# Kernel tuning notes

Measured on AMD Instinct MI355X. Metric: run time of the kernel, lower is better.

Reference implementation:

```python
import math
import jax, jax.numpy as jnp
import numpy as np

T, B, IN, H, D, ETA, R = 128, 32, 512, 8, 64, 4, 4
DE = ETA * D  # expanded key dim = eta * head_dim
EPS = 1e-05


def setup_inputs() -> dict:
    key = jax.random.key(0)
    ks = jax.random.split(key, 8)
    s = 0.05
    return {
        "inputs": jax.random.normal(ks[0], (T, B, IN), jnp.float32),
        "terminations": jnp.zeros((T, B), jnp.float32),
        "tilde_k_prev": jax.random.normal(ks[1], (B, R, H, DE), jnp.float32) * s,
        "tilde_v_prev": jax.random.normal(ks[2], (B, R, H, D), jnp.float32) * s,
        "s_prev": jax.random.normal(ks[3], (B, H, DE), jnp.float32) * s,
        "tick": jnp.zeros((B, 1), jnp.float32),
        "W_kqv": jax.random.normal(ks[4], (H * D * 5, IN), jnp.float32) * s,
        "b_kqv": jnp.zeros((H * D * 5,), jnp.float32),
        "W_p": jax.random.normal(ks[5], (H * ETA * 3, IN), jnp.float32) * s,
        "b_p": jnp.zeros((H * ETA * 3,), jnp.float32),
        "W_o": jax.random.normal(ks[6], (IN, H * D), jnp.float32) * s,
        "b_o": jnp.zeros((IN,), jnp.float32),
    }


def _forward(inputs, terminations, tilde_k_prev, tilde_v_prev, s_prev, tick,
             W_kqv, b_kqv, W_p, b_p, W_o, b_o):
    # projections
    kqv = (inputs @ W_kqv.T + b_kqv).reshape(T, B, H, 5, D)
    keys, queries, values, beta, gammas = (kqv[..., i, :] for i in range(5))
    p = (inputs @ W_p.T + b_p).reshape(T, B, H, 3, ETA)
    p1, p2, p3 = (p[..., i, :] for i in range(3))
    relu, sig = jax.nn.relu, jax.nn.sigmoid
    # kernel feature maps: outer product then flatten (d outer, n inner)
    keys = jnp.einsum('tbhd,tbhn->tbhdn', relu(keys), relu(p1)).reshape(T, B, H, DE)
    queries = jnp.einsum('tbhd,tbhn->tbhdn', relu(queries), relu(p2)).reshape(T, B, H, DE)
    gammas = jnp.einsum('tbhd,tbhn->tbhdn', sig(gammas), sig(p3)).reshape(T, B, H, DE)
    beta = sig(beta)  # (T,B,H,D)
    # oscillatory basis
    ticks = tick[None] + jnp.arange(1, T + 1, dtype=jnp.float32).reshape(T, 1, 1)  # (T,B,1)
    omegas = jnp.linspace(-math.pi, math.pi, R)
    occil = jnp.cos(ticks * omegas[None, None, :])  # (T,B,R)
    values = values * beta
    values_r = values[:, :, None] * occil[:, :, :, None, None]   # (T,B,R,H,D)
    keys_g = keys * gammas                                        # (T,B,H,DE)
    keys_r = keys_g[:, :, None] * occil[:, :, :, None, None]     # (T,B,R,H,DE)
    # discounts (with termination resets)
    nt = (1.0 - terminations)[:, :, None, None]
    dg = (1.0 - gammas) * nt  # (T,B,H,DE)
    db = (1.0 - beta) * nt    # (T,B,H,D)
    # recurrence y[t] = discount[t]*y[t-1] + x[t] via lax.scan over T
    def step(carry, xs):
        k_st, v_st, s_st = carry
        kx, vx, sx, dgt, dbt = xs
        k_new = dgt[:, None] * k_st + kx   # (B,R,H,DE)
        v_new = dbt[:, None] * v_st + vx   # (B,R,H,D)
        s_new = dgt * s_st + sx            # (B,H,DE)
        return (k_new, v_new, s_new), (k_new, v_new, s_new)
    (kf, vf, sf), (K, V, S) = jax.lax.scan(
        step, (tilde_k_prev, tilde_v_prev, s_prev), (keys_r, values_r, keys_g, dg, db))
    # attention readout
    kdq = jnp.einsum('tbrhd,tbhd->tbrh', K, queries)
    kv = jnp.einsum('tbrhd,tbrh->tbhd', V, kdq)
    norm = jnp.einsum('tbhd,tbhd->tbh', S, queries)
    attn = kv / (2 * R * norm[..., None] + EPS)  # (T,B,H,D)
    out = attn.reshape(T, B, H * D) @ W_o.T + b_o  # dropout p=0 (eval)
    return out, kf, vf, sf, tick + T


def reference(inputs, terminations, tilde_k_prev, tilde_v_prev, s_prev, tick,
              W_kqv, b_kqv, W_p, b_p, W_o, b_o):
    return _forward(inputs, terminations, tilde_k_prev, tilde_v_prev, s_prev, tick,
                    W_kqv, b_kqv, W_p, b_p, W_o, b_o)
```

## Files before the change

kernel.cpp:

```cpp
#include <hip/hip_runtime.h>
#include <math.h>
#include <stdint.h>

constexpr int T_ = 128, B_ = 32, IN_ = 512, H_ = 8, D_ = 64, ETA_ = 4, R_ = 4;
constexpr int DE_ = ETA_ * D_;
constexpr float EPS_ = 1e-5f;
constexpr int NKQV = H_ * 5 * D_;
constexpr int NP   = H_ * 3 * ETA_;
constexpr int M_   = T_ * B_;
constexpr int NCH  = 8;
constexpr int CH   = T_ / NCH;
constexpr int BH_  = B_ * H_;

typedef __attribute__((ext_vector_type(8))) short bf16x8;
typedef __attribute__((ext_vector_type(4))) float f32x4;

__device__ __forceinline__ float bf2f(unsigned short u) {
    return __builtin_bit_cast(float, ((unsigned)u) << 16);
}
__device__ __forceinline__ unsigned short f2bf(float f) {
    unsigned u = __builtin_bit_cast(unsigned, f);
    u = (u + 0x7fffu + ((u >> 16) & 1u)) >> 16;
    return (unsigned short)u;
}
__device__ __forceinline__ float fsigm(float x) {
    return __fdividef(1.f, 1.f + __expf(-x));
}

__global__ __launch_bounds__(256) void cast_f32_bf16(
    const float* __restrict__ src, unsigned short* __restrict__ dst, int n8)
{
    int i = blockIdx.x * 256 + threadIdx.x;
    if (i >= n8) return;
    const float4* s = (const float4*)src;
    float4 a = s[2 * i], b = s[2 * i + 1];
    *(ushort4*)(dst + 8 * i)     = make_ushort4(f2bf(a.x), f2bf(a.y), f2bf(a.z), f2bf(a.w));
    *(ushort4*)(dst + 8 * i + 4) = make_ushort4(f2bf(b.x), f2bf(b.y), f2bf(b.z), f2bf(b.w));
}

__global__ __launch_bounds__(256) void cast_split(
    const float* __restrict__ src, unsigned short* __restrict__ dst,
    int n4, int K3, int off_lo, int off_hi2)
{
    int i = blockIdx.x * 256 + threadIdx.x;
    if (i >= n4) return;
    const int r = i >> 7;
    const int c = (i & 127) << 2;
    float4 x = *(const float4*)(src + (size_t)r * 512 + c);
    ushort4 hi = make_ushort4(f2bf(x.x), f2bf(x.y), f2bf(x.z), f2bf(x.w));
    ushort4 lo = make_ushort4(f2bf(x.x - bf2f(hi.x)), f2bf(x.y - bf2f(hi.y)),
                              f2bf(x.z - bf2f(hi.z)), f2bf(x.w - bf2f(hi.w)));
    unsigned short* dr = dst + (size_t)r * K3 + c;
    *(ushort4*)dr = hi;
    *(ushort4*)(dr + off_lo) = lo;
    if (off_hi2 >= 0) *(ushort4*)(dr + off_hi2) = hi;
}

__device__ __forceinline__ void gl_lds16(const unsigned short* g, unsigned short* l) {
    __builtin_amdgcn_global_load_lds((const __attribute__((address_space(1))) void*)g,
                                     (__attribute__((address_space(3))) void*)l, 16, 0, 0);
}
__device__ __forceinline__ int ko_map(bool split, int ko) {
    return (split && ko >= 512) ? ko - 512 : ko;
}

template <bool SPLIT>
__global__ __launch_bounds__(256) void gemm_bf16(
    const unsigned short* __restrict__ A,
    const unsigned short* __restrict__ W,
    const float* __restrict__ bias1, const float* __restrict__ bias2,
    float* __restrict__ C1, float* __restrict__ C2,
    int M, int N1, int N2, int K, int sA, int sW)
{
    int bx, by;
    {
        const int nwg = gridDim.x * gridDim.y;
        int lin = blockIdx.y * gridDim.x + blockIdx.x;
        lin = (lin & 7) * (nwg >> 3) + (lin >> 3);
        const int G = (gridDim.x % 7 == 0) ? 7 : gridDim.x;
        const int grpsz = gridDim.y * G;
        const int cg = lin / grpsz, rem = lin % grpsz;
        by = rem / G;
        bx = cg * G + rem % G;
    }
    const int Ntot = N1 + N2;
    const int bm = by * 128;
    const int bn = bx * 128;
    const int tid = threadIdx.x;
    const int lane = tid & 63;
    const int wid = tid >> 6;
    const int wr = wid >> 1;
    const int wc = wid & 1;

    __shared__ __align__(16) unsigned short As[2][4096];
    __shared__ __align__(16) unsigned short Bs[2][4096];

    const int arow = tid & 127;
    const int akg  = tid >> 7;
    const unsigned short* aSrc = A + (size_t)(bm + arow) * sA + akg * 8;
    int wrow = bn + arow; if (wrow >= Ntot) wrow = 0;
    const unsigned short* bSrc = W + (size_t)wrow * sW + akg * 8;
    const int gb0 = (wid * 64) * 8;
    const int gb1 = (256 + wid * 64) * 8;

    const int fA = (((lane >> 4) * 128) + wr * 64 + (lane & 15)) * 8;
    const int fB = (((lane >> 4) * 128) + wc * 64 + (lane & 15)) * 8;

    f32x4 acc[4][4] = {};
    const int NKT = K >> 5;

    gl_lds16(aSrc, &As[0][gb0]);
    gl_lds16(aSrc + 16, &As[0][gb1]);
    gl_lds16(bSrc, &Bs[0][gb0]);
    gl_lds16(bSrc + 16, &Bs[0][gb1]);
    __syncthreads();

    for (int kt = 0; kt < NKT; ++kt) {
        const int cur = kt & 1;
        if (kt + 1 < NKT) {
            const int ko  = (kt + 1) << 5;
            const int koA = ko_map(SPLIT, ko);
            gl_lds16(aSrc + koA, &As[cur ^ 1][gb0]);
            gl_lds16(aSrc + koA + 16, &As[cur ^ 1][gb1]);
            gl_lds16(bSrc + ko, &Bs[cur ^ 1][gb0]);
            gl_lds16(bSrc + ko + 16, &Bs[cur ^ 1][gb1]);
        }
        bf16x8 af[4], bfr[4];
#pragma unroll
        for (int m = 0; m < 4; ++m) af[m] = *(const bf16x8*)&As[cur][fA + m * 128];
#pragma unroll
        for (int n = 0; n < 4; ++n) bfr[n] = *(const bf16x8*)&Bs[cur][fB + n * 128];
#pragma unroll
        for (int m = 0; m < 4; ++m)
#pragma unroll
            for (int n = 0; n < 4; ++n)
                acc[m][n] = __builtin_amdgcn_mfma_f32_16x16x32_bf16(af[m], bfr[n], acc[m][n], 0, 0, 0);
        __syncthreads();
    }

#pragma unroll
    for (int n = 0; n < 4; ++n) {
        const int col = bn + wc * 64 + n * 16 + (lane & 15);
        if (col < Ntot) {
            const float bv = (col < N1) ? bias1[col] : bias2[col - N1];
#pragma unroll
            for (int m = 0; m < 4; ++m) {
                const int row0 = bm + wr * 64 + m * 16 + ((lane >> 4) << 2);
#pragma unroll
                for (int j = 0; j < 4; ++j) {
                    const float v = acc[m][n][j] + bv;
                    const int row = row0 + j;
                    if (col < N1)
                        C1[(size_t)row * N1 + col] = v;
                    else
                        C2[(size_t)row * N2 + (col - N1)] = v;
                }
            }
        }
    }
}

template <int CTRL, int RM>
__device__ __forceinline__ float dpp_radd(float x) {
    int t = __builtin_amdgcn_update_dpp(0, __builtin_bit_cast(int, x), CTRL, RM, 0xf, true);
    return x + __builtin_bit_cast(float, t);
}
__device__ __forceinline__ float wave_allsum(float x) {
    x = dpp_radd<0x111, 0xf>(x);
    x = dpp_radd<0x112, 0xf>(x);
    x = dpp_radd<0x114, 0xf>(x);
    x = dpp_radd<0x118, 0xf>(x);
    x = dpp_radd<0x142, 0xa>(x);
    x = dpp_radd<0x143, 0xc>(x);
    return __builtin_bit_cast(float, __builtin_amdgcn_readlane(__builtin_bit_cast(int, x), 63));
}

__device__ __forceinline__ void osc2(float tt, float& oc03, float& oc12) {
    oc03 = cosf(3.14159265358979323846f * tt);
    oc12 = cosf(1.04719755119659774615f * tt);
}


__global__ __launch_bounds__(64) void scanA(
    const float* __restrict__ kqv, const float* __restrict__ pbuf,
    const float* __restrict__ term, const float* __restrict__ tick,
    float* __restrict__ Dg, float* __restrict__ Db,
    float* __restrict__ Kloc, float* __restrict__ Vloc, float* __restrict__ Sloc)
{
    const int bh = blockIdx.x & (BH_ - 1);
    const int c  = blockIdx.x >> 8;
    const int b = bh >> 3, h = bh & 7;
    const int d = threadIdx.x;

    float K0[4] = {}, K1[4] = {}, K2[4] = {}, K3[4] = {}, S[4] = {};
    float V0 = 0.f, V1 = 0.f, V2 = 0.f, V3 = 0.f;
    float Dgv[4] = {1.f, 1.f, 1.f, 1.f};
    float Dbv = 1.f;
    const float tk = tick[b];

    for (int t = c * CH; t < (c + 1) * CH; ++t) {
        const float* kq = kqv + ((size_t)t * B_ + b) * NKQV + h * 320;
        const float c0 = kq[d], c2 = kq[128 + d], c3 = kq[192 + d], c4 = kq[256 + d];
        const float* pr = pbuf + ((size_t)t * B_ + b) * NP + h * 12;
        const float4 p1 = *(const float4*)pr;
        const float4 p3 = *(const float4*)(pr + 8);
        const float nt = 1.f - term[(size_t)t * B_ + b];

        float oc03, oc12; osc2(tk + (float)(t + 1), oc03, oc12);
        const float sgam = fsigm(c4);
        const float rk = fmaxf(c0, 0.f);
        const float sbet = fsigm(c3);
        const float vb = c2 * sbet;
        const float dbv = (1.f - sbet) * nt;
        const float p1a[4] = {p1.x, p1.y, p1.z, p1.w};
        const float p3a[4] = {p3.x, p3.y, p3.z, p3.w};
#pragma unroll
        for (int n = 0; n < 4; ++n) {
            const float g  = sgam * fsigm(p3a[n]);
            const float kg = rk * fmaxf(p1a[n], 0.f) * g;
            const float dg = (1.f - g) * nt;
            S[n]  = fmaf(dg, S[n],  kg);
            K0[n] = fmaf(dg, K0[n], kg * oc03);
            K1[n] = fmaf(dg, K1[n], kg * oc12);
            K2[n] = fmaf(dg, K2[n], kg * oc12);
            K3[n] = fmaf(dg, K3[n], kg * oc03);
            Dgv[n] *= dg;
        }
        V0 = fmaf(dbv, V0, vb * oc03);
        V1 = fmaf(dbv, V1, vb * oc12);
        V2 = fmaf(dbv, V2, vb * oc12);
        V3 = fmaf(dbv, V3, vb * oc03);
        Dbv *= dbv;
    }

    const size_t cb = (size_t)c * BH_ + bh;
    *(float4*)&Dg[cb * DE_ + 4 * d] = make_float4(Dgv[0], Dgv[1], Dgv[2], Dgv[3]);
    Db[cb * D_ + d] = Dbv;
    *(float4*)&Kloc[(cb * 4 + 0) * DE_ + 4 * d] = make_float4(K0[0], K0[1], K0[2], K0[3]);
    *(float4*)&Kloc[(cb * 4 + 1) * DE_ + 4 * d] = make_float4(K1[0], K1[1], K1[2], K1[3]);
    *(float4*)&Kloc[(cb * 4 + 2) * DE_ + 4 * d] = make_float4(K2[0], K2[1], K2[2], K2[3]);
    *(float4*)&Kloc[(cb * 4 + 3) * DE_ + 4 * d] = make_float4(K3[0], K3[1], K3[2], K3[3]);
    Vloc[(cb * 4 + 0) * D_ + d] = V0;
    Vloc[(cb * 4 + 1) * D_ + d] = V1;
    Vloc[(cb * 4 + 2) * D_ + d] = V2;
    Vloc[(cb * 4 + 3) * D_ + d] = V3;
    *(float4*)&Sloc[cb * DE_ + 4 * d] = make_float4(S[0], S[1], S[2], S[3]);
}

__global__ __launch_bounds__(256) void scanB(
    const float* __restrict__ k_prev, const float* __restrict__ v_prev,
    const float* __restrict__ s_prev,
    float* __restrict__ Dg, float* __restrict__ Db,
    float* __restrict__ Kloc, float* __restrict__ Vloc, float* __restrict__ Sloc)
{
    const int bh = blockIdx.x;
    const int b = bh >> 3, h = bh & 7;
    const int de = threadIdx.x;

    float Kin[4], Sin, Vin[4];
#pragma unroll
    for (int r = 0; r < 4; ++r)
        Kin[r] = k_prev[((size_t)(b * 4 + r) * 8 + h) * DE_ + de];
    Sin = s_prev[((size_t)b * 8 + h) * DE_ + de];
    if (de < D_) {
#pragma unroll
        for (int r = 0; r < 4; ++r)
            Vin[r] = v_prev[((size_t)(b * 4 + r) * 8 + h) * D_ + de];
    }

    for (int c = 0; c < NCH; ++c) {
        const size_t cb = (size_t)c * BH_ + bh;
        const float dg = Dg[cb * DE_ + de];
#pragma unroll
        for (int r = 0; r < 4; ++r) {
            const size_t ix = (cb * 4 + r) * DE_ + de;
            const float kl = Kloc[ix];
            Kloc[ix] = Kin[r];
            Kin[r] = fmaf(dg, Kin[r], kl);
        }
        {
            const size_t ix = cb * DE_ + de;
            const float sl = Sloc[ix];
            Sloc[ix] = Sin;
            Sin = fmaf(dg, Sin, sl);
        }
        if (de < D_) {
            const float db = Db[cb * D_ + de];
#pragma unroll
            for (int r = 0; r < 4; ++r) {
                const size_t ix = (cb * 4 + r) * D_ + de;
                const float vl = Vloc[ix];
                Vloc[ix] = Vin[r];
                Vin[r] = fmaf(db, Vin[r], vl);
            }
        }
    }
}

__global__ __launch_bounds__(64) void scanC(
    const float* __restrict__ kqv, const float* __restrict__ pbuf,
    const float* __restrict__ term, const float* __restrict__ tick,
    const float* __restrict__ Kloc, const float* __restrict__ Vloc,
    const float* __restrict__ Sloc,
    unsigned short* __restrict__ attn,
    float* __restrict__ kf, float* __restrict__ vf, float* __restrict__ sf,
    float* __restrict__ tick_out)
{
    const int bh = blockIdx.x & (BH_ - 1);
    const int c  = blockIdx.x >> 8;
    const int b = bh >> 3, h = bh & 7;
    const int d = threadIdx.x;
    const size_t cb = (size_t)c * BH_ + bh;

    float K0[4], K1[4], K2[4], K3[4], S[4];
    float V0, V1, V2, V3;
    {
        float4 k4;
        k4 = *(const float4*)&Kloc[(cb * 4 + 0) * DE_ + 4 * d];
        K0[0] = k4.x; K0[1] = k4.y; K0[2] = k4.z; K0[3] = k4.w;
        k4 = *(const float4*)&Kloc[(cb * 4 + 1) * DE_ + 4 * d];
        K1[0] = k4.x; K1[1] = k4.y; K1[2] = k4.z; K1[3] = k4.w;
        k4 = *(const float4*)&Kloc[(cb * 4 + 2) * DE_ + 4 * d];
        K2[0] = k4.x; K2[1] = k4.y; K2[2] = k4.z; K2[3] = k4.w;
        k4 = *(const float4*)&Kloc[(cb * 4 + 3) * DE_ + 4 * d];
        K3[0] = k4.x; K3[1] = k4.y; K3[2] = k4.z; K3[3] = k4.w;
        k4 = *(const float4*)&Sloc[cb * DE_ + 4 * d];
        S[0] = k4.x; S[1] = k4.y; S[2] = k4.z; S[3] = k4.w;
        V0 = Vloc[(cb * 4 + 0) * D_ + d];
        V1 = Vloc[(cb * 4 + 1) * D_ + d];
        V2 = Vloc[(cb * 4 + 2) * D_ + d];
        V3 = Vloc[(cb * 4 + 3) * D_ + d];
    }
    const float tk = tick[b];

    for (int t = c * CH; t < (c + 1) * CH; ++t) {
        const float* kq = kqv + ((size_t)t * B_ + b) * NKQV + h * 320;
        const float c0 = kq[d], c1 = kq[64 + d], c2 = kq[128 + d],
                    c3 = kq[192 + d], c4 = kq[256 + d];
        const float* pr = pbuf + ((size_t)t * B_ + b) * NP + h * 12;
        const float4 p1 = *(const float4*)pr;
        const float4 p2 = *(const float4*)(pr + 4);
        const float4 p3 = *(const float4*)(pr + 8);
        const float nt = 1.f - term[(size_t)t * B_ + b];

        float oc03, oc12; osc2(tk + (float)(t + 1), oc03, oc12);
        const float sgam = fsigm(c4);
        const float rk = fmaxf(c0, 0.f);
        const float rq = fmaxf(c1, 0.f);
        const float sbet = fsigm(c3);
        const float vb = c2 * sbet;
        const float dbv = (1.f - sbet) * nt;
        const float p1a[4] = {p1.x, p1.y, p1.z, p1.w};
        const float p2a[4] = {p2.x, p2.y, p2.z, p2.w};
        const float p3a[4] = {p3.x, p3.y, p3.z, p3.w};

        float s0 = 0.f, s1 = 0.f, s2 = 0.f, s3 = 0.f, s4 = 0.f;
#pragma unroll
        for (int n = 0; n < 4; ++n) {
            const float g  = sgam * fsigm(p3a[n]);
            const float kg = rk * fmaxf(p1a[n], 0.f) * g;
            const float qe = rq * fmaxf(p2a[n], 0.f);
            const float dg = (1.f - g) * nt;
            S[n]  = fmaf(dg, S[n],  kg);
            K0[n] = fmaf(dg, K0[n], kg * oc03);
            K1[n] = fmaf(dg, K1[n], kg * oc12);
            K2[n] = fmaf(dg, K2[n], kg * oc12);
            K3[n] = fmaf(dg, K3[n], kg * oc03);
            s0 = fmaf(K0[n], qe, s0);
            s1 = fmaf(K1[n], qe, s1);
            s2 = fmaf(K2[n], qe, s2);
            s3 = fmaf(K3[n], qe, s3);
            s4 = fmaf(S[n],  qe, s4);
        }
        V0 = fmaf(dbv, V0, vb * oc03);
        V1 = fmaf(dbv, V1, vb * oc12);
        V2 = fmaf(dbv, V2, vb * oc12);
        V3 = fmaf(dbv, V3, vb * oc03);

        const float kdq0 = wave_allsum(s0);
        const float kdq1 = wave_allsum(s1);
        const float kdq2 = wave_allsum(s2);
        const float kdq3 = wave_allsum(s3);
        const float nrm  = wave_allsum(s4);

        const float kv = V0 * kdq0 + V1 * kdq1 + V2 * kdq2 + V3 * kdq3;
        attn[((size_t)t * B_ + b) * (H_ * D_) + h * D_ + d] =
            f2bf(__fdividef(kv, 2.f * (float)R_ * nrm + EPS_));
    }

    if (c == NCH - 1) {
        *(float4*)&kf[((size_t)(b * 4 + 0) * 8 + h) * DE_ + 4 * d] = make_float4(K0[0], K0[1], K0[2], K0[3]);
        *(float4*)&kf[((size_t)(b * 4 + 1) * 8 + h) * DE_ + 4 * d] = make_float4(K1[0], K1[1], K1[2], K1[3]);
        *(float4*)&kf[((size_t)(b * 4 + 2) * 8 + h) * DE_ + 4 * d] = make_float4(K2[0], K2[1], K2[2], K2[3]);
        *(float4*)&kf[((size_t)(b * 4 + 3) * 8 + h) * DE_ + 4 * d] = make_float4(K3[0], K3[1], K3[2], K3[3]);
        *(float4*)&sf[((size_t)b * 8 + h) * DE_ + 4 * d] = make_float4(S[0], S[1], S[2], S[3]);
        vf[((size_t)(b * 4 + 0) * 8 + h) * D_ + d] = V0;
        vf[((size_t)(b * 4 + 1) * 8 + h) * D_ + d] = V1;
        vf[((size_t)(b * 4 + 2) * 8 + h) * D_ + d] = V2;
        vf[((size_t)(b * 4 + 3) * 8 + h) * D_ + d] = V3;
        if (h == 0 && d == 0) tick_out[b] = tk + (float)T_;
    }
}

extern "C" void kernel_launch(void* const* d_in, const int* in_sizes, int n_in,
                              void* d_out, int out_size, void* d_ws, size_t ws_size,
                              hipStream_t stream)
{
    const float* inputs = (const float*)d_in[0];
    const float* term   = (const float*)d_in[1];
    const float* k_prev = (const float*)d_in[2];
    const float* v_prev = (const float*)d_in[3];
    const float* s_prev = (const float*)d_in[4];
    const float* tick   = (const float*)d_in[5];
    const float* W_kqv  = (const float*)d_in[6];
    const float* b_kqv  = (const float*)d_in[7];
    const float* W_p    = (const float*)d_in[8];
    const float* b_p    = (const float*)d_in[9];
    const float* W_o    = (const float*)d_in[10];
    const float* b_o    = (const float*)d_in[11];

    float* out = (float*)d_out;
    float* kf  = out + (size_t)T_ * B_ * IN_;
    float* vf  = kf  + (size_t)B_ * R_ * H_ * DE_;
    float* sf  = vf  + (size_t)B_ * R_ * H_ * D_;
    float* tick_out = sf + (size_t)B_ * H_ * DE_;

    float* kqv_f  = (float*)d_ws;
    float* p_f    = kqv_f + (size_t)M_ * NKQV;
    unsigned short* attn_bf = (unsigned short*)(p_f + (size_t)M_ * NP);
    unsigned short* Wo_bf   = attn_bf + (size_t)M_ * IN_;
    unsigned short* A2      = Wo_bf + (size_t)IN_ * (H_ * D_);
    unsigned short* W2      = A2 + (size_t)M_ * 1024;

    float* Dg   = (float*)A2;
    float* Db   = Dg   + (size_t)NCH * BH_ * DE_;
    float* Kloc = Db   + (size_t)NCH * BH_ * D_;
    float* Vloc = Kloc + (size_t)NCH * BH_ * 4 * DE_;
    float* Sloc = Vloc + (size_t)NCH * BH_ * 4 * D_;

    {
        int n4 = M_ * 128;
        cast_split<<<(n4 + 255) / 256, 256, 0, stream>>>(inputs, A2, n4, 1024, 512, -1);
        n4 = NKQV * 128;
        cast_split<<<(n4 + 255) / 256, 256, 0, stream>>>(W_kqv, W2, n4, 1536, 512, 1024);
        n4 = NP * 128;
        cast_split<<<(n4 + 255) / 256, 256, 0, stream>>>(W_p, W2 + (size_t)NKQV * 1536, n4, 1536, 512, 1024);
        int n8 = (IN_ * (H_ * D_)) / 8;
        cast_f32_bf16<<<(n8 + 255) / 256, 256, 0, stream>>>(W_o, Wo_bf, n8);
    }

    {
        dim3 grid((NKQV + NP + 127) / 128, M_ / 128);
        gemm_bf16<true><<<grid, 256, 0, stream>>>(A2, W2, b_kqv, b_p,
                                                  kqv_f, p_f, M_, NKQV, NP,
                                                  1536, 1024, 1536);
    }

    scanA<<<NCH * BH_, 64, 0, stream>>>(kqv_f, p_f, term, tick,
                                        Dg, Db, Kloc, Vloc, Sloc);
    scanB<<<BH_, 256, 0, stream>>>(k_prev, v_prev, s_prev,
                                   Dg, Db, Kloc, Vloc, Sloc);
    scanC<<<NCH * BH_, 64, 0, stream>>>(kqv_f, p_f, term, tick,
                                        Kloc, Vloc, Sloc, attn_bf,
                                        kf, vf, sf, tick_out);

    {
        dim3 grid(IN_ / 128, M_ / 128);
        gemm_bf16<false><<<grid, 256, 0, stream>>>(attn_bf, Wo_bf, b_o, b_o,
                                                   out, nullptr, M_, IN_, 0,
                                                   512, 512, 512);
    }
}
```

Measured before the change: 163.5 us.

## Permute projection weights so value/beta columns use single-pass bf16 GEMM

Reorders the kqv/p weight rows into one permuted matrix with a permuted bias, placing keys, queries, gammas and p first, then zero padding, then values and beta. Column tiles before the split column run the 3-term split-bf16 GEMM (K=1536), while value and beta tiles run plain bf16 (K=512). This cuts MFMA work for about 40% of the output columns and merges the two output buffers into one. Values and beta lose the hi/lo precision compensation, which risks accuracy.

```diff
diff --git a/kernel.cpp b/kernel.cpp
--- a/kernel.cpp
+++ b/kernel.cpp
@@ -5,13 +5,14 @@
 constexpr int T_ = 128, B_ = 32, IN_ = 512, H_ = 8, D_ = 64, ETA_ = 4, R_ = 4;
 constexpr int DE_ = ETA_ * D_;
 constexpr float EPS_ = 1e-5f;
-constexpr int NKQV = H_ * 5 * D_;
-constexpr int NP   = H_ * 3 * ETA_;
 constexpr int M_   = T_ * B_;
 constexpr int NCH  = 8;
 constexpr int CH   = T_ / NCH;
 constexpr int BH_  = B_ * H_;
 
+constexpr int NW = 2688;
+constexpr int SPLITCOL = 1664;
+
 typedef __attribute__((ext_vector_type(8))) short bf16x8;
 typedef __attribute__((ext_vector_type(4))) float f32x4;
 
@@ -27,20 +28,8 @@
     return __fdividef(1.f, 1.f + __expf(-x));
 }
 
-__global__ __launch_bounds__(256) void cast_f32_bf16(
-    const float* __restrict__ src, unsigned short* __restrict__ dst, int n8)
-{
-    int i = blockIdx.x * 256 + threadIdx.x;
-    if (i >= n8) return;
-    const float4* s = (const float4*)src;
-    float4 a = s[2 * i], b = s[2 * i + 1];
-    *(ushort4*)(dst + 8 * i)     = make_ushort4(f2bf(a.x), f2bf(a.y), f2bf(a.z), f2bf(a.w));
-    *(ushort4*)(dst + 8 * i + 4) = make_ushort4(f2bf(b.x), f2bf(b.y), f2bf(b.z), f2bf(b.w));
-}
-
-__global__ __launch_bounds__(256) void cast_split(
-    const float* __restrict__ src, unsigned short* __restrict__ dst,
-    int n4, int K3, int off_lo, int off_hi2)
+__global__ __launch_bounds__(256) void cast_splitA(
+    const float* __restrict__ src, unsigned short* __restrict__ dst, int n4)
 {
     int i = blockIdx.x * 256 + threadIdx.x;
     if (i >= n4) return;
@@ -50,27 +39,79 @@
     ushort4 hi = make_ushort4(f2bf(x.x), f2bf(x.y), f2bf(x.z), f2bf(x.w));
     ushort4 lo = make_ushort4(f2bf(x.x - bf2f(hi.x)), f2bf(x.y - bf2f(hi.y)),
                               f2bf(x.z - bf2f(hi.z)), f2bf(x.w - bf2f(hi.w)));
-    unsigned short* dr = dst + (size_t)r * K3 + c;
+    unsigned short* dr = dst + (size_t)r * 1024 + c;
     *(ushort4*)dr = hi;
-    *(ushort4*)(dr + off_lo) = lo;
-    if (off_hi2 >= 0) *(ushort4*)(dr + off_hi2) = hi;
+    *(ushort4*)(dr + 512) = lo;
+}
+
+__global__ __launch_bounds__(256) void build_w2_bias(
+    const float* __restrict__ Wkqv, const float* __restrict__ Wp,
+    const float* __restrict__ bkqv, const float* __restrict__ bp,
+    unsigned short* __restrict__ W2, float* __restrict__ bias_perm)
+{
+    int i = blockIdx.x * 256 + threadIdx.x;
+    if (i >= NW * 128) return;
+    const int rr = i >> 7;
+    const int c = (i & 127) << 2;
+
+    bool zero = false;
+    const float* srow = nullptr;
+    float bv = 0.f;
+    if (rr < 512) {
+        const int h = rr >> 6, dd = rr & 63, s = h * 320 + dd;
+        srow = Wkqv + (size_t)s * 512; bv = bkqv[s];
+    } else if (rr < 1024) {
+        const int q = rr - 512, h = q >> 6, dd = q & 63, s = h * 320 + 64 + dd;
+        srow = Wkqv + (size_t)s * 512; bv = bkqv[s];
+    } else if (rr < 1536) {
+        const int q = rr - 1024, h = q >> 6, dd = q & 63, s = h * 320 + 256 + dd;
+        srow = Wkqv + (size_t)s * 512; bv = bkqv[s];
+    } else if (rr < 1632) {
+        const int q = rr - 1536;
+        srow = Wp + (size_t)q * 512; bv = bp[q];
+    } else if (rr < 1664) {
+        zero = true;
+    } else if (rr < 2176) {
+        const int q = rr - 1664, h = q >> 6, dd = q & 63, s = h * 320 + 128 + dd;
+        srow = Wkqv + (size_t)s * 512; bv = bkqv[s];
+    } else {
+        const int q = rr - 2176, h = q >> 6, dd = q & 63, s = h * 320 + 192 + dd;
+        srow = Wkqv + (size_t)s * 512; bv = bkqv[s];
+    }
+
+    float4 x = zero ? make_float4(0.f, 0.f, 0.f, 0.f) : *(const float4*)(srow + c);
+    ushort4 hi = make_ushort4(f2bf(x.x), f2bf(x.y), f2bf(x.z), f2bf(x.w));
+    ushort4 lo = make_ushort4(f2bf(x.x - bf2f(hi.x)), f2bf(x.y - bf2f(hi.y)),
+                              f2bf(x.z - bf2f(hi.z)), f2bf(x.w - bf2f(hi.w)));
+    unsigned short* dr = W2 + (size_t)rr * 1536 + c;
+    *(ushort4*)dr = hi;
+    *(ushort4*)(dr + 512) = lo;
+    *(ushort4*)(dr + 1024) = hi;
+    if (c == 0) bias_perm[rr] = zero ? 0.f : bv;
+}
+
+__global__ __launch_bounds__(256) void cast_f32_bf16(
+    const float* __restrict__ src, unsigned short* __restrict__ dst, int n8)
+{
+    int i = blockIdx.x * 256 + threadIdx.x;
+    if (i >= n8) return;
+    const float4* s = (const float4*)src;
+    float4 a = s[2 * i], b = s[2 * i + 1];
+    *(ushort4*)(dst + 8 * i)     = make_ushort4(f2bf(a.x), f2bf(a.y), f2bf(a.z), f2bf(a.w));
+    *(ushort4*)(dst + 8 * i + 4) = make_ushort4(f2bf(b.x), f2bf(b.y), f2bf(b.z), f2bf(b.w));
 }
 
 __device__ __forceinline__ void gl_lds16(const unsigned short* g, unsigned short* l) {
     __builtin_amdgcn_global_load_lds((const __attribute__((address_space(1))) void*)g,
                                      (__attribute__((address_space(3))) void*)l, 16, 0, 0);
 }
-__device__ __forceinline__ int ko_map(bool split, int ko) {
-    return (split && ko >= 512) ? ko - 512 : ko;
-}
-
-template <bool SPLIT>
+
 __global__ __launch_bounds__(256) void gemm_bf16(
     const unsigned short* __restrict__ A,
     const unsigned short* __restrict__ W,
-    const float* __restrict__ bias1, const float* __restrict__ bias2,
-    float* __restrict__ C1, float* __restrict__ C2,
-    int M, int N1, int N2, int K, int sA, int sW)
+    const float* __restrict__ bias,
+    float* __restrict__ C,
+    int N, int sA, int sW, int kBig, int kSmall, int splitcol)
 {
     int bx, by;
     {
@@ -83,7 +124,6 @@
         by = rem / G;
         bx = cg * G + rem % G;
     }
-    const int Ntot = N1 + N2;
     const int bm = by * 128;
     const int bn = bx * 128;
     const int tid = threadIdx.x;
@@ -98,8 +138,7 @@
     const int arow = tid & 127;
     const int akg  = tid >> 7;
     const unsigned short* aSrc = A + (size_t)(bm + arow) * sA + akg * 8;
-    int wrow = bn + arow; if (wrow >= Ntot) wrow = 0;
-    const unsigned short* bSrc = W + (size_t)wrow * sW + akg * 8;
+    const unsigned short* bSrc = W + (size_t)(bn + arow) * sW + akg * 8;
     const int gb0 = (wid * 64) * 8;
     const int gb1 = (256 + wid * 64) * 8;
 
@@ -107,6 +146,7 @@
     const int fB = (((lane >> 4) * 128) + wc * 64 + (lane & 15)) * 8;
 
     f32x4 acc[4][4] = {};
+    const int K = (bn < splitcol) ? kBig : kSmall;
     const int NKT = K >> 5;
 
     gl_lds16(aSrc, &As[0][gb0]);
@@ -119,7 +159,7 @@
         const int cur = kt & 1;
         if (kt + 1 < NKT) {
             const int ko  = (kt + 1) << 5;
-            const int koA = ko_map(SPLIT, ko);
+            const int koA = (ko >= 512) ? ko - 512 : ko;
             gl_lds16(aSrc + koA, &As[cur ^ 1][gb0]);
             gl_lds16(aSrc + koA + 16, &As[cur ^ 1][gb1]);
             gl_lds16(bSrc + ko, &Bs[cur ^ 1][gb0]);
@@ -141,21 +181,13 @@
 #pragma unroll
     for (int n = 0; n < 4; ++n) {
         const int col = bn + wc * 64 + n * 16 + (lane & 15);
-        if (col < Ntot) {
-            const float bv = (col < N1) ? bias1[col] : bias2[col - N1];
-#pragma unroll
-            for (int m = 0; m < 4; ++m) {
-                const int row0 = bm + wr * 64 + m * 16 + ((lane >> 4) << 2);
-#pragma unroll
-                for (int j = 0; j < 4; ++j) {
-                    const float v = acc[m][n][j] + bv;
-                    const int row = row0 + j;
-                    if (col < N1)
-                        C1[(size_t)row * N1 + col] = v;
-                    else
-                        C2[(size_t)row * N2 + (col - N1)] = v;
-                }
-            }
+        const float bv = bias[col];
+#pragma unroll
+        for (int m = 0; m < 4; ++m) {
+            const int row0 = bm + wr * 64 + m * 16 + ((lane >> 4) << 2);
+#pragma unroll
+            for (int j = 0; j < 4; ++j)
+                C[(size_t)(row0 + j) * N + col] = acc[m][n][j] + bv;
         }
     }
 }
@@ -182,8 +214,8 @@
 
 
 __global__ __launch_bounds__(64) void scanA(
-    const float* __restrict__ kqv, const float* __restrict__ pbuf,
-    const float* __restrict__ term, const float* __restrict__ tick,
+    const float* __restrict__ kqv, const float* __restrict__ term,
+    const float* __restrict__ tick,
     float* __restrict__ Dg, float* __restrict__ Db,
     float* __restrict__ Kloc, float* __restrict__ Vloc, float* __restrict__ Sloc)
 {
@@ -199,9 +231,12 @@
     const float tk = tick[b];
 
     for (int t = c * CH; t < (c + 1) * CH; ++t) {
-        const float* kq = kqv + ((size_t)t * B_ + b) * NKQV + h * 320;
-        const float c0 = kq[d], c2 = kq[128 + d], c3 = kq[192 + d], c4 = kq[256 + d];
-        const float* pr = pbuf + ((size_t)t * B_ + b) * NP + h * 12;
+        const float* row = kqv + ((size_t)t * B_ + b) * NW;
+        const float c0 = row[h * 64 + d];
+        const float c2 = row[1664 + h * 64 + d];
+        const float c3 = row[2176 + h * 64 + d];
+        const float c4 = row[1024 + h * 64 + d];
+        const float* pr = row + 1536 + h * 12;
         const float4 p1 = *(const float4*)pr;
         const float4 p3 = *(const float4*)(pr + 8);
         const float nt = 1.f - term[(size_t)t * B_ + b];
@@ -298,8 +333,8 @@
 }
 
 __global__ __launch_bounds__(64) void scanC(
-    const float* __restrict__ kqv, const float* __restrict__ pbuf,
-    const float* __restrict__ term, const float* __restrict__ tick,
+    const float* __restrict__ kqv, const float* __restrict__ term,
+    const float* __restrict__ tick,
     const float* __restrict__ Kloc, const float* __restrict__ Vloc,
     const float* __restrict__ Sloc,
     unsigned short* __restrict__ attn,
@@ -334,10 +369,13 @@
     const float tk = tick[b];
 
     for (int t = c * CH; t < (c + 1) * CH; ++t) {
-        const float* kq = kqv + ((size_t)t * B_ + b) * NKQV + h * 320;
-        const float c0 = kq[d], c1 = kq[64 + d], c2 = kq[128 + d],
-                    c3 = kq[192 + d], c4 = kq[256 + d];
-        const float* pr = pbuf + ((size_t)t * B_ + b) * NP + h * 12;
+        const float* row = kqv + ((size_t)t * B_ + b) * NW;
+        const float c0 = row[h * 64 + d];
+        const float c1 = row[512 + h * 64 + d];
+        const float c2 = row[1664 + h * 64 + d];
+        const float c3 = row[2176 + h * 64 + d];
+        const float c4 = row[1024 + h * 64 + d];
+        const float* pr = row + 1536 + h * 12;
         const float4 p1 = *(const float4*)pr;
         const float4 p2 = *(const float4*)(pr + 4);
         const float4 p3 = *(const float4*)(pr + 8);
@@ -425,12 +463,12 @@
     float* sf  = vf  + (size_t)B_ * R_ * H_ * D_;
     float* tick_out = sf + (size_t)B_ * H_ * DE_;
 
-    float* kqv_f  = (float*)d_ws;
-    float* p_f    = kqv_f + (size_t)M_ * NKQV;
-    unsigned short* attn_bf = (unsigned short*)(p_f + (size_t)M_ * NP);
+    float* kqv_s = (float*)d_ws;
+    unsigned short* attn_bf = (unsigned short*)(kqv_s + (size_t)M_ * NW);
     unsigned short* Wo_bf   = attn_bf + (size_t)M_ * IN_;
     unsigned short* A2      = Wo_bf + (size_t)IN_ * (H_ * D_);
     unsigned short* W2      = A2 + (size_t)M_ * 1024;
+    float* bias_perm        = (float*)(W2 + (size_t)NW * 1536);
 
     float* Dg   = (float*)A2;
     float* Db   = Dg   + (size_t)NCH * BH_ * DE_;
@@ -440,34 +478,28 @@
 
     {
         int n4 = M_ * 128;
-        cast_split<<<(n4 + 255) / 256, 256, 0, stream>>>(inputs, A2, n4, 1024, 512, -1);
-        n4 = NKQV * 128;
-        cast_split<<<(n4 + 255) / 256, 256, 0, stream>>>(W_kqv, W2, n4, 1536, 512, 1024);
-        n4 = NP * 128;
-        cast_split<<<(n4 + 255) / 256, 256, 0, stream>>>(W_p, W2 + (size_t)NKQV * 1536, n4, 1536, 512, 1024);
+        cast_splitA<<<(n4 + 255) / 256, 256, 0, stream>>>(inputs, A2, n4);
+        n4 = NW * 128;
+        build_w2_bias<<<(n4 + 255) / 256, 256, 0, stream>>>(W_kqv, W_p, b_kqv, b_p,
+                                                            W2, bias_perm);
         int n8 = (IN_ * (H_ * D_)) / 8;
         cast_f32_bf16<<<(n8 + 255) / 256, 256, 0, stream>>>(W_o, Wo_bf, n8);
     }
 
     {
-        dim3 grid((NKQV + NP + 127) / 128, M_ / 128);
-        gemm_bf16<true><<<grid, 256, 0, stream>>>(A2, W2, b_kqv, b_p,
-                                                  kqv_f, p_f, M_, NKQV, NP,
-                                                  1536, 1024, 1536);
-    }
-
-    scanA<<<NCH * BH_, 64, 0, stream>>>(kqv_f, p_f, term, tick,
-                                        Dg, Db, Kloc, Vloc, Sloc);
-    scanB<<<BH_, 256, 0, stream>>>(k_prev, v_prev, s_prev,
-                                   Dg, Db, Kloc, Vloc, Sloc);
-    scanC<<<NCH * BH_, 64, 0, stream>>>(kqv_f, p_f, term, tick,
-                                        Kloc, Vloc, Sloc, attn_bf,
-                                        kf, vf, sf, tick_out);
+        dim3 grid(NW / 128, M_ / 128);
+        gemm_bf16<<<grid, 256, 0, stream>>>(A2, W2, bias_perm, kqv_s,
+                                            NW, 1024, 1536, 1536, 512, SPLITCOL);
+    }
+
+    scanA<<<NCH * BH_, 64, 0, stream>>>(kqv_s, term, tick, Dg, Db, Kloc, Vloc, Sloc);
+    scanB<<<BH_, 256, 0, stream>>>(k_prev, v_prev, s_prev, Dg, Db, Kloc, Vloc, Sloc);
+    scanC<<<NCH * BH_, 64, 0, stream>>>(kqv_s, term, tick, Kloc, Vloc, Sloc,
+                                        attn_bf, kf, vf, sf, tick_out);
 
     {
         dim3 grid(IN_ / 128, M_ / 128);
-        gemm_bf16<false><<<grid, 256, 0, stream>>>(attn_bf, Wo_bf, b_o, b_o,
-                                                   out, nullptr, M_, IN_, 0,
-                                                   512, 512, 512);
-    }
-}
+        gemm_bf16<<<grid, 256, 0, stream>>>(attn_bf, Wo_bf, b_o, out,
+                                            IN_, 512, 512, 512, 512, 0);
+    }
+}
```

Result: faster. 159.7 us (-2.3%).
